# Optimization experiments

Measured on AMD Instinct MI355X. Metric: run time of the kernel, lower is better.

The kernel has to match this reference:

```python
import jax, jax.numpy as jnp
import numpy as np
import math

RADIUS = 1.0
PERCENTAGES = (0.02, 0.04, 0.06, 0.08, 0.10)


def _fps(pts, npoint):
    """Furthest point sampling. pts: [N,3] -> idx [npoint] int32 (starts at index 0,
    matching pointnet2 CUDA furthest_point_sample)."""
    N = pts.shape[0]

    def step(carry, _):
        dists, last = carry
        d = jnp.sum((pts - pts[last]) ** 2, axis=-1)
        dists = jnp.minimum(dists, d)
        nxt = jnp.argmax(dists).astype(jnp.int32)
        return (dists, nxt), nxt

    init = (jnp.full((N,), 1e10, pts.dtype), jnp.int32(0))
    _, rest = jax.lax.scan(step, init, None, length=npoint - 1)
    return jnp.concatenate([jnp.zeros((1,), jnp.int32), rest])


def _ball_query(pcd, queries, r, nsample):
    """pcd [B,N,3], queries [B,M,3] -> idx [B,M,nsample] int32.
    First (by index order) points with squared dist < r^2; groups with fewer than
    nsample in-radius points are padded with the first found index (pn2 semantics)."""
    N = pcd.shape[1]
    d2 = jnp.sum((queries[:, :, None, :] - pcd[:, None, :, :]) ** 2, axis=-1)  # [B,M,N]
    key = jnp.where(d2 < r * r, jnp.arange(N, dtype=jnp.int32), jnp.int32(N))
    srt = jnp.sort(key, axis=-1)[:, :, :nsample]  # first in-radius indices
    valid = srt < N
    first = jnp.where(srt[:, :, :1] < N, srt[:, :, :1], 0)
    return jnp.where(valid, srt, first)


def _nn_dist(g):
    """g [G,n,3] -> [G,n] distance to nearest neighbor (2nd-smallest pairwise
    Euclidean distance, i.e. KNN(k=2) dist[:,:,1] including self-distance 0)."""
    sq = jnp.sum(g * g, axis=-1)  # [G,n]
    d2 = sq[:, :, None] + sq[:, None, :] - 2.0 * jnp.einsum('gnc,gmc->gnm', g, g)
    d2 = jnp.maximum(d2, 0.0)
    # safe sqrt (zero grad at exact zeros: self / duplicated padded points)
    d = jnp.where(d2 > 0, jnp.sqrt(jnp.where(d2 > 0, d2, 1.0)), 0.0)
    neg2, _ = jax.lax.top_k(-d, 2)  # two smallest distances
    return -neg2[:, :, 1]


def _uniform_loss(pcd):
    B, N, C = pcd.shape
    npoint = int(N * 0.05)
    fps_idx = jax.vmap(_fps, in_axes=(0, None))(pcd, npoint)  # [B,M]
    new_xyz = jnp.take_along_axis(pcd, fps_idx[:, :, None], axis=1)  # [B,M,3]
    loss = jnp.zeros((), pcd.dtype)
    for p in PERCENTAGES:
        nsample = int(N * p)
        r = math.sqrt(p * RADIUS)
        disk_area = math.pi * RADIUS ** 2 / N
        expect_len = math.sqrt(disk_area)
        idx = _ball_query(pcd, new_xyz, r, nsample)  # [B,M,n]
        grouped = jax.vmap(lambda pts, ii: pts[ii])(pcd, idx)  # [B,M,n,3]
        g = grouped.reshape(B * npoint, nsample, C)
        nn = _nn_dist(g)  # [G,n]
        e_ = 0.1
        u = jnp.abs(nn + e_)
        u = jnp.mean(u, axis=1)  # [G]
        u = (u - expect_len) ** 2 / (expect_len + e_)
        loss = loss + jnp.mean(u) * (p * 100.0) ** 2
    return loss / len(PERCENTAGES)


def setup_inputs() -> dict:
    key = jax.random.key(0)
    pcd = jax.random.uniform(key, (2, 4096, 3), dtype=jnp.float32)
    return {"pcd": pcd}


def reference(pcd):
    return _uniform_loss(pcd)
```

## Files before the change

### kernel.cpp

```cpp
#include <hip/hip_runtime.h>
#include <cmath>

#define NPTS 4096
#define NPOINT 204
#define NPCT 5
#define MAXNS 409
#define FPS_T 512
#define NGROUP 408
#define NPART (NGROUP * NPCT)
#define MAXSLOT 7
#define NWAVE 8

#define NWORK  510
#define NROUND 4

#define SMEM_BYTES 65664
#define KEYS_OFF   65536
#define WRES_OFF   6544
#define WTOT_OFF   35216
#define SPART_OFF  35248
#define SQI_OFF    35280

typedef unsigned long long u64;
typedef float f32x2 __attribute__((ext_vector_type(2)));

struct LossParams {
    int   nsample[NPCT];
    float r2[NPCT];
    float wscale[NPCT];
    float expect_len;
};

template <int CTRL>
__device__ __forceinline__ int dpp_imax(int v) {
    int t = __builtin_amdgcn_update_dpp(0, v, CTRL, 0xf, 0xf, true);
    return v > t ? v : t;
}
template <int CTRL>
__device__ __forceinline__ int dpp_imin(int v) {
    int t = __builtin_amdgcn_update_dpp(0x7fffffff, v, CTRL, 0xf, 0xf, false);
    return v < t ? v : t;
}
__device__ __forceinline__ int wave_max_i(int v) {
    v = dpp_imax<0x111>(v); v = dpp_imax<0x112>(v);
    v = dpp_imax<0x114>(v); v = dpp_imax<0x118>(v);
    v = dpp_imax<0x142>(v); v = dpp_imax<0x143>(v);
    return __builtin_amdgcn_readlane(v, 63);
}
__device__ __forceinline__ int wave_min_i(int v) {
    v = dpp_imin<0x111>(v); v = dpp_imin<0x112>(v);
    v = dpp_imin<0x114>(v); v = dpp_imin<0x118>(v);
    v = dpp_imin<0x142>(v); v = dpp_imin<0x143>(v);
    return __builtin_amdgcn_readlane(v, 63);
}
template <int CTRL>
__device__ __forceinline__ u64 dpp_u64max(u64 v) {
    int lo = (int)(unsigned)v;
    int hi = (int)(unsigned)(v >> 32);
    unsigned slo = (unsigned)__builtin_amdgcn_update_dpp(0, lo, CTRL, 0xf, 0xf, true);
    unsigned shi = (unsigned)__builtin_amdgcn_update_dpp(0, hi, CTRL, 0xf, 0xf, true);
    u64 o = ((u64)shi << 32) | slo;
    return v > o ? v : o;
}

__device__ void fps_role(const float* __restrict__ pcd,
                         int* __restrict__ fps_idx,
                         char* smem) {
#pragma clang fp contract(off)
    __builtin_amdgcn_s_setprio(3);
    float4* pts = reinterpret_cast<float4*>(smem);
    u64 (*keys)[NWAVE] = reinterpret_cast<u64 (*)[NWAVE]>(smem + KEYS_OFF);

    const int b = blockIdx.x;
    const int t = threadIdx.x;
    const int wave = t >> 6, lane = t & 63;
    const float* base = pcd + (size_t)b * NPTS * 3;

    f32x2 X[4], Y[4], Z[4], D[4];
    #pragma unroll
    for (int q = 0; q < 4; ++q) {
        int n0 = (2 * q) * FPS_T + t;
        int n1 = (2 * q + 1) * FPS_T + t;
        float x0 = base[3 * n0 + 0], y0 = base[3 * n0 + 1], z0 = base[3 * n0 + 2];
        float x1 = base[3 * n1 + 0], y1 = base[3 * n1 + 1], z1 = base[3 * n1 + 2];
        pts[n0] = make_float4(x0, y0, z0, 0.0f);
        pts[n1] = make_float4(x1, y1, z1, 0.0f);
        X[q] = (f32x2){x0, x1};
        Y[q] = (f32x2){y0, y1};
        Z[q] = (f32x2){z0, z1};
        D[q] = (f32x2){1e10f, 1e10f};
    }
    int* out = fps_idx + b * NPOINT;
    if (t == 0)
        __hip_atomic_store(&out[0], 0, __ATOMIC_RELAXED, __HIP_MEMORY_SCOPE_AGENT);
    __syncthreads();

    float4 c = pts[0];
    for (int it = 1; it < NPOINT; ++it) {
        f32x2 cxx = (f32x2){c.x, c.x};
        f32x2 cyy = (f32x2){c.y, c.y};
        f32x2 czz = (f32x2){c.z, c.z};
        int bb = -1, bi = 0;
        #pragma unroll
        for (int q = 0; q < 4; ++q) {
            f32x2 dx = X[q] - cxx, dy = Y[q] - cyy, dz = Z[q] - czz;
            f32x2 d  = (dx * dx + dy * dy) + dz * dz;
            f32x2 dd = D[q];
            float d0 = fminf(dd.x, d.x);
            float d1 = fminf(dd.y, d.y);
            D[q] = (f32x2){d0, d1};
            int b0 = __float_as_int(d0);
            int b1 = __float_as_int(d1);
            if (b0 > bb) { bb = b0; bi = (2 * q) * FPS_T + t; }
            if (b1 > bb) { bb = b1; bi = (2 * q + 1) * FPS_T + t; }
        }
        int wmax = wave_max_i(bb);
        int cand = (bb == wmax) ? bi : 0x7fffffff;
        int widx = wave_min_i(cand);
        if (lane == 0)
            keys[it & 1][wave] =
                ((u64)(unsigned)wmax << 32) | (unsigned)~(unsigned)widx;
        asm volatile("s_waitcnt lgkmcnt(0)" ::: "memory");
        __builtin_amdgcn_s_barrier();
        u64 kv = keys[it & 1][lane & 7];
        kv = dpp_u64max<0x111>(kv);
        kv = dpp_u64max<0x112>(kv);
        kv = dpp_u64max<0x114>(kv);
        unsigned lo7 = (unsigned)__builtin_amdgcn_readlane((int)(unsigned)kv, 7);
        int last = (int)~lo7;
        c = pts[last];
        if (t == 0)
            __hip_atomic_store(&out[it], last, __ATOMIC_RELAXED, __HIP_MEMORY_SCOPE_AGENT);
    }
}

template <int K>
__device__ __forceinline__ void phaseB(const float4* __restrict__ gpts,
                                       float2 (*wres)[64],
                                       int j0, int j1, int lane, int cntB) {
    float4 pi[K];
    float m1[K], m2[K];
    #pragma unroll
    for (int s = 0; s < K; ++s) {
        int idx = s * 64 + lane;
        pi[s] = gpts[idx < cntB ? idx : 0];
        m1[s] = 1e30f; m2[s] = 1e30f;
    }
    #pragma unroll 2
    for (int j = j0; j < j1; ++j) {
        float4 a = gpts[j];
        #pragma unroll
        for (int s = 0; s < K; ++s) {
            float tt = pi[s].x * a.x;
            tt = fmaf(pi[s].y, a.y, tt);
            tt = fmaf(pi[s].z, a.z, tt);
            float h = fmaf(-2.0f, tt, a.w);
            m2[s] = __builtin_amdgcn_fmed3f(m1[s], m2[s], h);
            m1[s] = fminf(m1[s], h);
        }
    }
    #pragma unroll
    for (int s = 0; s < K; ++s) wres[s][lane] = (float2){m1[s], m2[s]};
}

__device__ __forceinline__ float2 min2merge(float2 a, float2 b) {
    return (float2){fminf(a.x, b.x),
                    fminf(fmaxf(a.x, b.x), fminf(a.y, b.y))};
}

__device__ void worker_role(const float* __restrict__ pcd,
                            int* __restrict__ fps_idx,
                            float* __restrict__ partials,
                            const LossParams& P, char* smem) {
    float4* gpts = reinterpret_cast<float4*>(smem);
    auto wres    = reinterpret_cast<float2 (*)[MAXSLOT][64]>(smem + WRES_OFF);
    int*   s_wtot = reinterpret_cast<int*>(smem + WTOT_OFF);
    float* s_part = reinterpret_cast<float*>(smem + SPART_OFF);
    int*   s_qi   = reinterpret_cast<int*>(smem + SQI_OFF);

    const int w = blockIdx.x - 2;
    const int t = threadIdx.x;
    const int wave = t >> 6, lane = t & 63;

    for (int round = 0; round < NROUND; ++round) {
        const int tau  = w + round * NWORK;
        const int m_   = tau / 10;
        const int rem  = tau - m_ * 10;
        const int b    = rem / 5;
        const int pidx = rem - b * 5;

        const int   ns = P.nsample[pidx];
        const float r2 = P.r2[pidx];
        const float* base = pcd + (size_t)b * NPTS * 3;

        if (t == 0) {
            int q;
            while ((q = __hip_atomic_load(&fps_idx[b * NPOINT + m_],
                                          __ATOMIC_RELAXED,
                                          __HIP_MEMORY_SCOPE_AGENT)) < 0)
                __builtin_amdgcn_s_sleep(16);
            s_qi[0] = q;
        }
        __syncthreads();
        const int qi = s_qi[0];
        float qx = base[3 * qi + 0], qy = base[3 * qi + 1], qz = base[3 * qi + 2];

        unsigned long long msk[8];
        int lbase[8];
        int run = 0;
        #pragma unroll 4
        for (int s = 0; s < 8; ++s) {
            int n = wave * 512 + s * 64 + lane;
            float x = base[3 * n + 0];
            float y = base[3 * n + 1];
            float z = base[3 * n + 2];
            float d2;
            {
#pragma clang fp contract(off)
                float dx = qx - x, dy = qy - y, dz = qz - z;
                float aa = dx * dx, bb2 = dy * dy, cc = dz * dz;
                d2 = (aa + bb2) + cc;
            }
            msk[s] = __ballot(d2 < r2);
            lbase[s] = run;
            run += __popcll(msk[s]);
        }
        if (lane == 0) s_wtot[wave] = run;
        __syncthreads();
        int Bw = 0, cnt = 0;
        #pragma unroll
        for (int j = 0; j < NWAVE; ++j) {
            int wj = s_wtot[j];
            cnt += wj;
            if (j < wave) Bw += wj;
        }
        int cntB = cnt < ns ? cnt : ns;
        const int npad = ns - cntB;

        #pragma unroll 4
        for (int s = 0; s < 8; ++s) {
            int gb = Bw + lbase[s];
            if (gb >= ns) break;
            unsigned long long mk = msk[s];
            bool in = (mk >> lane) & 1ull;
            int pos = gb + __popcll(mk & ((1ull << lane) - 1ull));
            if (in && pos < ns) {
                int n = wave * 512 + s * 64 + lane;
                float x = base[3 * n], y = base[3 * n + 1], z = base[3 * n + 2];
                float sq = fmaf(x, x, fmaf(y, y, z * z));
                gpts[pos] = make_float4(x, y, z, sq);
            }
        }
        __syncthreads();

        const int eighth = (cntB + 7) >> 3;
        const int j0 = wave * eighth;
        const int j1 = (j0 + eighth) < cntB ? (j0 + eighth) : cntB;
        const int nslot = (cntB + 63) >> 6;
        switch (nslot) {
            case 1: phaseB<1>(gpts, wres[wave], j0, j1, lane, cntB); break;
            case 2: phaseB<2>(gpts, wres[wave], j0, j1, lane, cntB); break;
            case 3: phaseB<3>(gpts, wres[wave], j0, j1, lane, cntB); break;
            case 4: phaseB<4>(gpts, wres[wave], j0, j1, lane, cntB); break;
            case 5: phaseB<5>(gpts, wres[wave], j0, j1, lane, cntB); break;
            case 6: phaseB<6>(gpts, wres[wave], j0, j1, lane, cntB); break;
            default: phaseB<7>(gpts, wres[wave], j0, j1, lane, cntB); break;
        }
        __syncthreads();

        float sum = 0.0f;
        for (int it = t; it < nslot * 64; it += FPS_T) {
            int i = it;
            if (i < cntB) {
                int s = it >> 6, l = it & 63;
                float2 e  = min2merge(wres[0][s][l], wres[1][s][l]);
                float2 f  = min2merge(wres[2][s][l], wres[3][s][l]);
                float2 g  = min2merge(wres[4][s][l], wres[5][s][l]);
                float2 h  = min2merge(wres[6][s][l], wres[7][s][l]);
                float2 ef = min2merge(e, f);
                float2 gh = min2merge(g, h);
                float m2v = fminf(fmaxf(ef.x, gh.x), fminf(ef.y, gh.y));
                float sq = gpts[i].w;
                float d2 = fmaxf(sq + m2v, 0.0f);
                if (!(i == 0 && npad > 0)) sum += sqrtf(d2);
            }
        }
        #pragma unroll
        for (int off = 32; off; off >>= 1) sum += __shfl_down(sum, off);
        if (lane == 0) s_part[wave] = sum;
        __syncthreads();
        if (t == 0) {
            float tot = 0.0f;
            #pragma unroll
            for (int j = 0; j < NWAVE; ++j) tot += s_part[j];
            tot += 0.1f * (float)ns;
            float u  = tot / (float)ns;
            float du = u - P.expect_len;
            partials[tau] = du * du / (P.expect_len + 0.1f) * P.wscale[pidx];
        }
    }
}

__global__ __launch_bounds__(FPS_T, 4) void fused_kernel(const float* __restrict__ pcd,
                                                         int* __restrict__ fps_idx,
                                                         float* __restrict__ partials,
                                                         LossParams P) {
    __shared__ __align__(16) char smem[SMEM_BYTES];
    if (blockIdx.x < 2) {
        fps_role(pcd, fps_idx, smem);
    } else {
        worker_role(pcd, fps_idx, partials, P, smem);
    }
}

__global__ __launch_bounds__(256) void reduce_kernel(const float* __restrict__ partials,
                                                     float* __restrict__ out) {
    const int t = threadIdx.x;
    __shared__ float sp[4];
    float s = 0.0f;
    for (int i = t; i < NPART; i += 256) s += partials[i];
    #pragma unroll
    for (int off = 32; off; off >>= 1) s += __shfl_down(s, off);
    if ((t & 63) == 0) sp[t >> 6] = s;
    __syncthreads();
    if (t == 0) out[0] = sp[0] + sp[1] + sp[2] + sp[3];
}

extern "C" void kernel_launch(void* const* d_in, const int* in_sizes, int n_in,
                              void* d_out, int out_size, void* d_ws, size_t ws_size,
                              hipStream_t stream) {
    const float* pcd = (const float*)d_in[0];
    const int B = in_sizes[0] / (NPTS * 3);
    float* out = (float*)d_out;
    int*   fps = (int*)d_ws;
    float* partials = (float*)d_ws + NGROUP;

    hipMemsetAsync(fps, 0xFF, NGROUP * sizeof(int), stream);

    LossParams P;
    const double ps[NPCT] = {0.02, 0.04, 0.06, 0.08, 0.10};
    for (int i = 0; i < NPCT; ++i) {
        P.nsample[i] = (int)(NPTS * ps[i]);
        double r = std::sqrt(ps[i] * 1.0);
        P.r2[i] = (float)(r * r);
        double w = (ps[i] * 100.0) * (ps[i] * 100.0);
        P.wscale[i] = (float)(w / (double)(B * NPOINT * NPCT));
    }
    P.expect_len = (float)std::sqrt(3.14159265358979323846 / (double)NPTS);

    fused_kernel<<<dim3(2 + NWORK), dim3(FPS_T), 0, stream>>>(pcd, fps, partials, P);
    reduce_kernel<<<dim3(1), dim3(256), 0, stream>>>(partials, out);
}
```

Measured before the change: 185.4 us.

## Fuse final reduction into main kernel and drop memset via self-resetting globals

Removes the separate hipMemsetAsync and reduce_kernel launch by storing FPS indices bitwise-inverted in a device global that the last finishing worker block resets to zero, and by having that last block (found via an atomic counter) sum the partials. The grid shrinks from 512 to 256 blocks so all blocks are co-resident (launch bounds relaxed to 2 blocks per CU, larger shared buffer), with each worker handling 8 rounds plus an extra task for the first 8 workers. This cuts launch and memset overhead, but each worker now does twice as many sequential tasks, which may lengthen the critical path.

```diff
diff --git a/kernel.cpp b/kernel.cpp
--- a/kernel.cpp
+++ b/kernel.cpp
@@ -11,10 +11,11 @@
 #define MAXSLOT 7
 #define NWAVE 8
 
-#define NWORK  510
-#define NROUND 4
-
-#define SMEM_BYTES 65664
+#define NBLOCKS 256
+#define NWORK   254
+#define NROUND  8
+
+#define SMEM_BYTES 83968
 #define KEYS_OFF   65536
 #define WRES_OFF   6544
 #define WTOT_OFF   35216
@@ -30,6 +31,9 @@
     float wscale[NPCT];
     float expect_len;
 };
+
+__device__ int g_fps[NGROUP];
+__device__ int g_done;
 
 template <int CTRL>
 __device__ __forceinline__ int dpp_imax(int v) {
@@ -63,9 +67,7 @@
     return v > o ? v : o;
 }
 
-__device__ void fps_role(const float* __restrict__ pcd,
-                         int* __restrict__ fps_idx,
-                         char* smem) {
+__device__ void fps_role(const float* __restrict__ pcd, char* smem) {
 #pragma clang fp contract(off)
     __builtin_amdgcn_s_setprio(3);
     float4* pts = reinterpret_cast<float4*>(smem);
@@ -90,9 +92,9 @@
         Z[q] = (f32x2){z0, z1};
         D[q] = (f32x2){1e10f, 1e10f};
     }
-    int* out = fps_idx + b * NPOINT;
+    int* out = g_fps + b * NPOINT;
     if (t == 0)
-        __hip_atomic_store(&out[0], 0, __ATOMIC_RELAXED, __HIP_MEMORY_SCOPE_AGENT);
+        __hip_atomic_store(&out[0], ~0, __ATOMIC_RELAXED, __HIP_MEMORY_SCOPE_AGENT);
     __syncthreads();
 
     float4 c = pts[0];
@@ -130,7 +132,7 @@
         int last = (int)~lo7;
         c = pts[last];
         if (t == 0)
-            __hip_atomic_store(&out[it], last, __ATOMIC_RELAXED, __HIP_MEMORY_SCOPE_AGENT);
+            __hip_atomic_store(&out[it], ~last, __ATOMIC_RELAXED, __HIP_MEMORY_SCOPE_AGENT);
     }
 }
 
@@ -169,21 +171,20 @@
 }
 
 __device__ void worker_role(const float* __restrict__ pcd,
-                            int* __restrict__ fps_idx,
                             float* __restrict__ partials,
-                            const LossParams& P, char* smem) {
+                            float* __restrict__ out,
+                            const LossParams& P, char* smem, int w) {
     float4* gpts = reinterpret_cast<float4*>(smem);
     auto wres    = reinterpret_cast<float2 (*)[MAXSLOT][64]>(smem + WRES_OFF);
     int*   s_wtot = reinterpret_cast<int*>(smem + WTOT_OFF);
     float* s_part = reinterpret_cast<float*>(smem + SPART_OFF);
     int*   s_qi   = reinterpret_cast<int*>(smem + SQI_OFF);
 
-    const int w = blockIdx.x - 2;
     const int t = threadIdx.x;
     const int wave = t >> 6, lane = t & 63;
 
-    for (int round = 0; round < NROUND; ++round) {
-        const int tau  = w + round * NWORK;
+    for (int round = (w < 8 ? -1 : 0); round < NROUND; ++round) {
+        const int tau  = (round < 0) ? w : 8 + w + round * NWORK;
         const int m_   = tau / 10;
         const int rem  = tau - m_ * 10;
         const int b    = rem / 5;
@@ -194,12 +195,12 @@
         const float* base = pcd + (size_t)b * NPTS * 3;
 
         if (t == 0) {
-            int q;
-            while ((q = __hip_atomic_load(&fps_idx[b * NPOINT + m_],
+            int v;
+            while ((v = __hip_atomic_load(&g_fps[b * NPOINT + m_],
                                           __ATOMIC_RELAXED,
-                                          __HIP_MEMORY_SCOPE_AGENT)) < 0)
+                                          __HIP_MEMORY_SCOPE_AGENT)) >= 0)
                 __builtin_amdgcn_s_sleep(16);
-            s_qi[0] = q;
+            s_qi[0] = ~v;
         }
         __syncthreads();
         const int qi = s_qi[0];
@@ -298,44 +299,50 @@
             float du = u - P.expect_len;
             partials[tau] = du * du / (P.expect_len + 0.1f) * P.wscale[pidx];
         }
-    }
-}
-
-__global__ __launch_bounds__(FPS_T, 4) void fused_kernel(const float* __restrict__ pcd,
-                                                         int* __restrict__ fps_idx,
+        __syncthreads();
+    }
+
+    if (t == 0) {
+        int old = __hip_atomic_fetch_add(&g_done, 1, __ATOMIC_ACQ_REL,
+                                         __HIP_MEMORY_SCOPE_AGENT);
+        s_qi[0] = old;
+    }
+    __syncthreads();
+    if (s_qi[0] == NWORK - 1) {
+        (void)__hip_atomic_load(&g_done, __ATOMIC_ACQUIRE, __HIP_MEMORY_SCOPE_AGENT);
+        float s = 0.0f;
+        if (t < 256) {
+            for (int i = t; i < NPART; i += 256) s += partials[i];
+        }
+        #pragma unroll
+        for (int off = 32; off; off >>= 1) s += __shfl_down(s, off);
+        if (t < 256 && (t & 63) == 0) s_part[t >> 6] = s;
+        __syncthreads();
+        if (t == 0) out[0] = s_part[0] + s_part[1] + s_part[2] + s_part[3];
+        for (int i = t; i < NGROUP; i += FPS_T) g_fps[i] = 0;
+        if (t == 0) g_done = 0;
+    }
+}
+
+__global__ __launch_bounds__(FPS_T, 2) void fused_kernel(const float* __restrict__ pcd,
                                                          float* __restrict__ partials,
+                                                         float* __restrict__ out,
                                                          LossParams P) {
     __shared__ __align__(16) char smem[SMEM_BYTES];
-    if (blockIdx.x < 2) {
-        fps_role(pcd, fps_idx, smem);
+    const int bid = blockIdx.x;
+    if (bid < 2) {
+        fps_role(pcd, smem);
     } else {
-        worker_role(pcd, fps_idx, partials, P, smem);
-    }
-}
-
-__global__ __launch_bounds__(256) void reduce_kernel(const float* __restrict__ partials,
-                                                     float* __restrict__ out) {
-    const int t = threadIdx.x;
-    __shared__ float sp[4];
-    float s = 0.0f;
-    for (int i = t; i < NPART; i += 256) s += partials[i];
-    #pragma unroll
-    for (int off = 32; off; off >>= 1) s += __shfl_down(s, off);
-    if ((t & 63) == 0) sp[t >> 6] = s;
-    __syncthreads();
-    if (t == 0) out[0] = sp[0] + sp[1] + sp[2] + sp[3];
+        worker_role(pcd, partials, out, P, smem, bid - 2);
+    }
 }
 
 extern "C" void kernel_launch(void* const* d_in, const int* in_sizes, int n_in,
                               void* d_out, int out_size, void* d_ws, size_t ws_size,
                               hipStream_t stream) {
     const float* pcd = (const float*)d_in[0];
-    const int B = in_sizes[0] / (NPTS * 3);
     float* out = (float*)d_out;
-    int*   fps = (int*)d_ws;
-    float* partials = (float*)d_ws + NGROUP;
-
-    hipMemsetAsync(fps, 0xFF, NGROUP * sizeof(int), stream);
+    float* partials = (float*)d_ws;
 
     LossParams P;
     const double ps[NPCT] = {0.02, 0.04, 0.06, 0.08, 0.10};
@@ -344,10 +351,9 @@
         double r = std::sqrt(ps[i] * 1.0);
         P.r2[i] = (float)(r * r);
         double w = (ps[i] * 100.0) * (ps[i] * 100.0);
-        P.wscale[i] = (float)(w / (double)(B * NPOINT * NPCT));
+        P.wscale[i] = (float)(w / (double)(2 * NPOINT * NPCT));
     }
     P.expect_len = (float)std::sqrt(3.14159265358979323846 / (double)NPTS);
 
-    fused_kernel<<<dim3(2 + NWORK), dim3(FPS_T), 0, stream>>>(pcd, fps, partials, P);
-    reduce_kernel<<<dim3(1), dim3(256), 0, stream>>>(partials, out);
-}
+    fused_kernel<<<dim3(NBLOCKS), dim3(FPS_T), 0, stream>>>(pcd, partials, out, P);
+}
```

After: 194.7 us. 5.0% more time.
